# Kernel optimization log

Hardware: AMD Instinct MI355X
Metric: run time of the kernel (lower is better)

## Reference

```python
import jax, jax.numpy as jnp
import numpy as np
from jax import lax

CUTOFF = 0.25
SIGMA = 1.0
RADIUS = 4  # skimage/scipy default truncate=4.0 -> radius = round(4.0*sigma)


def _gauss_kernel(sigma=SIGMA, radius=RADIUS):
    x = np.arange(-radius, radius + 1, dtype=np.float32)
    k = np.exp(-0.5 * (x / sigma) ** 2)
    return jnp.asarray(k / k.sum())


def _blur_axis(x, axis, kernel):
    r = (kernel.shape[0] - 1) // 2
    pad = [(0, 0)] * x.ndim
    pad[axis] = (r, r)
    xp = jnp.pad(x, pad, mode='edge')  # scipy mode='nearest'
    out = jnp.zeros_like(x)
    for i in range(kernel.shape[0]):  # fixed small tap loop (9 taps)
        out = out + kernel[i] * lax.slice_in_dim(xp, i, i + x.shape[axis], axis=axis)
    return out


def gaussian_smoothing_4d(x):
    # skimage.filters.gaussian on a 4D array smooths over ALL axes (B, C, H, W)
    k = _gauss_kernel().astype(x.dtype)
    for ax in range(4):
        x = _blur_axis(x, ax, k)
    return x


def dht_2d(x):
    # real(FFT(x)) - imag(FFT(flip(x)))
    return (jnp.fft.fftn(x, axes=(2, 3)).real
            - jnp.fft.fftn(jnp.flip(x, axis=(2, 3)), axes=(2, 3)).imag).astype(x.dtype)


def _neg_k(a):
    # X_H(-k): flip both spatial mode axes, then roll by 1 (DC stays put)
    return jnp.roll(jnp.flip(a, axis=(-2, -1)), shift=(1, 1), axis=(-2, -1))


def compl_mul2d(x1, x2):
    x1n, x2n = _neg_k(x1), _neg_k(x2)
    e = lambda a, b: jnp.einsum('bixy,ioxy->boxy', a, b)
    return 0.5 * (e(x1, x2) - e(x1n, x2n) + e(x1, x2n) + e(x1n, x2))


def setup_inputs() -> dict:
    key = jax.random.key(0)
    k1, k2 = jax.random.split(key)
    B, Cin, Cout, H, W, M1, M2 = 16, 64, 64, 128, 128, 20, 20
    x = jax.random.normal(k1, (B, Cin, H, W), dtype=jnp.float32)
    scale = 1.0 / (Cin * Cout)
    w1 = scale * jax.random.uniform(k2, (Cin, Cout, M1, M2), dtype=jnp.float32)
    return {'x': x, 'w1': w1}


def reference(x, w1):
    B, _, H, W = x.shape
    Cout, M1, M2 = w1.shape[1], w1.shape[2], w1.shape[3]
    x_ht = dht_2d(x)
    out_ht = jnp.zeros((B, Cout, H, W), dtype=x.dtype)
    out_ht = out_ht.at[:, :, :M1, :M2].set(
        compl_mul2d(x_ht[:, :, :M1, :M2], w1))
    # inverse DHT = DHT / (H*W)
    y = dht_2d(out_ht) / (H * W)
    y = gaussian_smoothing_4d(y)
    # low-pass mask along last dim only (as in the original)
    freqs = jnp.fft.fftfreq(W)
    mask = (jnp.abs(freqs) <= CUTOFF).astype(y.dtype)
    return y * mask
```

## Files before the change

kernel.cpp:

```cpp
#include <hip/hip_runtime.h>


#define TWO_PI 6.283185307179586f
#define THETA (TWO_PI / 128.0f)

__device__ __forceinline__ void gauss9(float* g) {
  float s = 0.f;
#pragma unroll
  for (int t = 0; t < 9; ++t) { float d = (float)(t - 4); g[t] = expf(-0.5f * d * d); s += g[t]; }
  float inv = 1.f / s;
#pragma unroll
  for (int t = 0; t < 9; ++t) g[t] *= inv;
}

__global__ void __launch_bounds__(256, 4) kBig(
    const float* __restrict__ x, const float* __restrict__ w1,
    float* __restrict__ X1, float* __restrict__ wbT,
    float* __restrict__ L2g, float* __restrict__ RB2g) {
  __shared__ float lds[10240];
  int tid = threadIdx.x;
  int blk = blockIdx.x;

  if (blk >= 1024) {
    if (blk == 1472) {
      for (int i = tid; i < 5376; i += 256) {
        int u = i / 42, t = i - u * 42;
        int A = (t < 21) ? t : t - 21;
        float a = (float)((u * A) & 127) * THETA;
        lds[u * 44 + t] = (t < 21) ? cosf(a) : sinf(a);
      }
      __syncthreads();
      float g[9]; gauss9(g);
      for (int i = tid; i < 5376; i += 256) {
        int u = i / 42, t = i - u * 42;
        float acc = 0.f;
#pragma unroll
        for (int tp = 0; tp < 9; ++tp) {
          int uc = u - 4 + tp; uc = uc < 0 ? 0 : (uc > 127 ? 127 : uc);
          acc += g[tp] * lds[uc * 44 + t];
        }
        L2g[t * 128 + u] = acc;
        bool keep = (u <= 32) || (u >= 96);
        RB2g[t * 128 + u] = keep ? acc : 0.f;
      }
      return;
    }
    int bb = blk - 1024;
    int c = bb / 7, chunk = bb % 7;
    int m0 = chunk * 64;
    int mw = 400 - m0; if (mw > 64) mw = 64;
    for (int t = tid; t < 4096; t += 256) {
      int o = t >> 6, mm = t & 63;
      lds[o * 69 + mm] = (mm < mw) ? w1[(c * 64 + o) * 400 + m0 + mm] : 0.f;
    }
    __syncthreads();
    float g[9]; gauss9(g);
    for (int t = tid; t < 4096; t += 256) {
      int mm = t >> 6, o = t & 63;
      if (mm >= mw) continue;
      float acc = 0.f;
#pragma unroll
      for (int tp = 0; tp < 9; ++tp) {
        int oc = o - 4 + tp; oc = oc < 0 ? 0 : (oc > 63 ? 63 : oc);
        acc += g[tp] * lds[oc * 69 + mm];
      }
      wbT[(c * 400 + m0 + mm) * 64 + o] = acc;
    }
    return;
  }

  int bc = blk;
  const float* xb = x + (long)bc * 16384;

  for (int i = tid; i < 2600; i += 256) {
    int n2 = i / 40, col = i - n2 * 40;
    int k2 = (col < 20) ? col : col - 20;
    float s, c;
    sincosf((float)((k2 * n2) & 127) * THETA, &s, &c);
    lds[i] = (col < 20) ? c : s;
  }

  int rg = tid & 31, cg = tid >> 5;
  int r0 = rg * 4, c0 = cg * 5;
  float acc[4][5];
#pragma unroll
  for (int i = 0; i < 4; ++i)
#pragma unroll
    for (int j = 0; j < 5; ++j) acc[i][j] = 0.f;

  float* xsP = lds + 2600;
  float* xsM = lds + 4844;
  const float* xsrc = (cg < 4) ? xsP : xsM;

  for (int ch = 0; ch < 4; ++ch) {
    __syncthreads();
#pragma unroll
    for (int it = 0; it < 2; ++it) {
      int t = tid + it * 256;
      int n2l = t & 15, n1g = t >> 4;
      int base = ch * 16 + n2l;
      const float* gp = xb + n1g * 512 + base;
      float a0 = gp[0], a1 = gp[128], a2 = gp[256], a3 = gp[384];
      float b0 = 0.f, b1 = 0.f, b2 = 0.f, b3 = 0.f;
      if (base != 0) {
        const float* gm = xb + n1g * 512 + (128 - base);
        b0 = gm[0]; b1 = gm[128]; b2 = gm[256]; b3 = gm[384];
      }
      *(float4*)&xsP[n2l * 132 + n1g * 4] =
          make_float4(a0 + b0, a1 + b1, a2 + b2, a3 + b3);
      *(float4*)&xsM[n2l * 132 + n1g * 4] =
          make_float4(a0 - b0, a1 - b1, a2 - b2, a3 - b3);
    }
    if (ch == 3 && tid < 32) {
      int n1g = tid;
      const float* gp = xb + n1g * 512 + 64;
      float4 v = make_float4(gp[0], gp[128], gp[256], gp[384]);
      *(float4*)&xsP[16 * 132 + n1g * 4] = v;
      *(float4*)&xsM[16 * 132 + n1g * 4] = v;
    }
    __syncthreads();
#pragma unroll 4
    for (int k = 0; k < 16; ++k) {
      float4 av = *(const float4*)&xsrc[k * 132 + r0];
      const float* tr = lds + (ch * 16 + k) * 40 + c0;
      float bv[5] = {tr[0], tr[1], tr[2], tr[3], tr[4]};
      float avv[4] = {av.x, av.y, av.z, av.w};
#pragma unroll
      for (int i = 0; i < 4; ++i)
#pragma unroll
        for (int j = 0; j < 5; ++j) acc[i][j] += avv[i] * bv[j];
    }
    if (ch == 3) {
      float4 av = *(const float4*)&xsrc[16 * 132 + r0];
      const float* tr = lds + 64 * 40 + c0;
      float bv[5] = {tr[0], tr[1], tr[2], tr[3], tr[4]};
      float avv[4] = {av.x, av.y, av.z, av.w};
#pragma unroll
      for (int i = 0; i < 4; ++i)
#pragma unroll
        for (int j = 0; j < 5; ++j) acc[i][j] += avv[i] * bv[j];
    }
  }
  __syncthreads();
  for (int i = tid; i < 2560; i += 256) {
    int k1 = i >> 7, t = i & 127;
    float s, c;
    sincosf((float)((k1 * t) & 127) * THETA, &s, &c);
    lds[k1 * 128 + (t ^ ((k1 & 7) << 2))] = c;
    lds[(20 + k1) * 128 + (t ^ (((20 + k1) & 7) << 2))] = s;
  }
#pragma unroll
  for (int j = 0; j < 5; ++j) {
    int col = c0 + j;
    int k2 = (col < 20) ? col : col - 20;
    int part = (col < 20) ? 0 : 128;
    int m = (k2 & 7) << 2;
    *(float4*)&lds[5120 + k2 * 256 + ((part + r0) ^ m)] =
        make_float4(acc[0][j], acc[1][j], acc[2][j], acc[3][j]);
  }
  __syncthreads();
  if (tid < 200) {
    int k1 = tid / 10, k2 = (tid % 10) * 2;
    int mc = (k1 & 7) << 2, ms = ((20 + k1) & 7) << 2;
    int m0 = (k2 & 7) << 2, m1 = ((k2 + 1) & 7) << 2;
    const float* tgc = lds + k1 * 128;
    const float* tgs = lds + (20 + k1) * 128;
    const float* p0 = lds + 5120 + k2 * 256;
    const float* p1 = lds + 5120 + (k2 + 1) * 256;
    float Ac0 = 0.f, As0 = 0.f, Bc0 = 0.f, Bs0 = 0.f;
    float Ac1 = 0.f, As1 = 0.f, Bc1 = 0.f, Bs1 = 0.f;
    for (int t = 0; t < 128; t += 4) {
      float4 tc = *(const float4*)(tgc + (t ^ mc));
      float4 ts = *(const float4*)(tgs + (t ^ ms));
      float4 pc0 = *(const float4*)(p0 + (t ^ m0));
      float4 ps0 = *(const float4*)(p0 + 128 + (t ^ m0));
      float4 pc1 = *(const float4*)(p1 + (t ^ m1));
      float4 ps1 = *(const float4*)(p1 + 128 + (t ^ m1));
      Ac0 += tc.x*pc0.x + tc.y*pc0.y + tc.z*pc0.z + tc.w*pc0.w;
      As0 += ts.x*pc0.x + ts.y*pc0.y + ts.z*pc0.z + ts.w*pc0.w;
      Bc0 += tc.x*ps0.x + tc.y*ps0.y + tc.z*ps0.z + tc.w*ps0.w;
      Bs0 += ts.x*ps0.x + ts.y*ps0.y + ts.z*ps0.z + ts.w*ps0.w;
      Ac1 += tc.x*pc1.x + tc.y*pc1.y + tc.z*pc1.z + tc.w*pc1.w;
      As1 += ts.x*pc1.x + ts.y*pc1.y + ts.z*pc1.z + ts.w*pc1.w;
      Bc1 += tc.x*ps1.x + tc.y*ps1.y + tc.z*ps1.z + tc.w*ps1.w;
      Bs1 += ts.x*ps1.x + ts.y*ps1.y + ts.z*ps1.z + ts.w*ps1.w;
    }
    float sa, ca, sb, cb;
    sincosf(THETA * (float)(k1 + k2), &sa, &ca);
    sincosf(THETA * (float)(k1 + k2 + 1), &sb, &cb);
    X1[(k1 * 20 + k2) * 1024 + bc] = (Ac0 - Bs0) * (1.f - sa) - (As0 + Bc0) * ca;
    X1[(k1 * 20 + k2 + 1) * 1024 + bc] = (Ac1 - Bs1) * (1.f - sb) - (As1 + Bc1) * cb;
  }
}

__global__ void k3_mix(const float* __restrict__ X1, const float* __restrict__ wbT,
                       float* __restrict__ O) {
  __shared__ float Xp[16][64], Xm[16][64];
  int m = blockIdx.x;
  int i = m / 20, j = m - i * 20;
  int nm = ((20 - i) % 20) * 20 + ((20 - j) % 20);
  int tid = threadIdx.x;
  const float sc = 0.5f / 16384.0f;
  float g[9]; gauss9(g);
  {
    int bl = tid >> 6, c = tid & 63;
#pragma unroll
    for (int it = 0; it < 4; ++it) {
      int b = bl * 4 + it;
      float sa = 0.f, sn = 0.f;
#pragma unroll
      for (int tp = 0; tp < 9; ++tp) {
        int bb = b - 4 + tp; bb = bb < 0 ? 0 : (bb > 15 ? 15 : bb);
        sa += g[tp] * X1[m * 1024 + bb * 64 + c];
        sn += g[tp] * X1[nm * 1024 + bb * 64 + c];
      }
      Xp[b][c] = (sa + sn) * sc; Xm[b][c] = (sa - sn) * sc;
    }
  }
  __syncthreads();
  int o = tid & 63, bq = tid >> 6;
  float acc[4] = {0.f, 0.f, 0.f, 0.f};
#pragma unroll 4
  for (int c = 0; c < 64; ++c) {
    float wp = wbT[(c * 400 + m) * 64 + o];
    float wm = wbT[(c * 400 + nm) * 64 + o];
#pragma unroll
    for (int k = 0; k < 4; ++k)
      acc[k] += Xp[bq * 4 + k][c] * wp + Xm[bq * 4 + k][c] * wm;
  }
#pragma unroll
  for (int k = 0; k < 4; ++k)
    O[((bq * 4 + k) * 64 + o) * 400 + m] = acc[k];
}

__global__ void __launch_bounds__(256) k5b_final(const float* __restrict__ O,
                                                 const float* __restrict__ L2g,
                                                 const float* __restrict__ RB2g,
                                                 float* __restrict__ out) {
  __shared__ float Os[400];
  __shared__ float Rs[42 * 128];
  int bo = blockIdx.x, tid = threadIdx.x;
  for (int t = tid; t < 400; t += 256) Os[t] = O[bo * 400 + t];
  __syncthreads();
  const float4* Bc4 = (const float4*)RB2g;
  const float4* Bs4 = (const float4*)(RB2g + 21 * 128);
  {
    int rg = tid & 7;
    int vqIdx = tid >> 3;
    int vq = (vqIdx < 9) ? vqIdx : vqIdx + 15;
    if (rg < 7 && vqIdx < 17) {
      int r0 = rg * 6;
      float4 a[6];
#pragma unroll
      for (int q = 0; q < 6; ++q) a[q] = make_float4(0.f, 0.f, 0.f, 0.f);
      for (int k2 = 0; k2 <= 20; ++k2) {
        float4 bc4 = Bc4[k2 * 32 + vq];
        float4 bs4 = Bs4[k2 * 32 + vq];
#pragma unroll
        for (int q = 0; q < 6; ++q) {
          int r = r0 + q;
          bool isS = (r >= 21);
          int A = isS ? (r - 21) : r;
          if (k2 < 20 && A < 20) {
            float ov = Os[A * 20 + k2];
            const float4 b = isS ? bs4 : bc4;
            float s = isS ? -ov : ov;
            a[q].x += s * b.x; a[q].y += s * b.y; a[q].z += s * b.z; a[q].w += s * b.w;
          }
          if (k2 >= 1 && A >= 1) {
            float ov = Os[(A - 1) * 20 + (k2 - 1)];
            const float4 b = isS ? bc4 : bs4;
            a[q].x -= ov * b.x; a[q].y -= ov * b.y; a[q].z -= ov * b.z; a[q].w -= ov * b.w;
          }
        }
      }
#pragma unroll
      for (int q = 0; q < 6; ++q)
        *(float4*)&Rs[(r0 + q) * 128 + vq * 4] = a[q];
    }
  }
  __syncthreads();
  long base = (long)bo * 16384;
  {
    int half = tid >> 7;
    int uu = (tid >> 3) & 15;  int u0 = uu * 8;
    int vv = tid & 7;          int v0 = half ? (96 + vv * 4) : vv * 4;
    float acc[8][4];
#pragma unroll
    for (int a = 0; a < 8; ++a)
#pragma unroll
      for (int b = 0; b < 4; ++b) acc[a][b] = 0.f;
    for (int r = 0; r < 42; ++r) {
      float4 a0 = *(const float4*)(L2g + r * 128 + u0);
      float4 a1 = *(const float4*)(L2g + r * 128 + u0 + 4);
      float4 b0 = *(const float4*)&Rs[r * 128 + v0];
      float av[8] = {a0.x, a0.y, a0.z, a0.w, a1.x, a1.y, a1.z, a1.w};
      float bv[4] = {b0.x, b0.y, b0.z, b0.w};
#pragma unroll
      for (int a = 0; a < 8; ++a)
#pragma unroll
        for (int b = 0; b < 4; ++b) acc[a][b] += av[a] * bv[b];
    }
#pragma unroll
    for (int a = 0; a < 8; ++a)
      *(float4*)&out[base + (u0 + a) * 128 + v0] =
          make_float4(acc[a][0], acc[a][1], acc[a][2], acc[a][3]);
  }
  if (tid < 128) {
    float d = 0.f;
    for (int r = 0; r < 42; ++r) d += L2g[r * 128 + tid] * Rs[r * 128 + 32];
    out[base + tid * 128 + 32] = d;
  }
  float4 z4 = make_float4(0.f, 0.f, 0.f, 0.f);
  for (int jj = tid; jj < 2048; jj += 256) {
    int u = jj >> 4, s = jj & 15;
    long p = base + (long)u * 128;
    if (s == 15) { out[p + 33] = 0.f; out[p + 34] = 0.f; out[p + 35] = 0.f; }
    else *(float4*)&out[p + 36 + 4 * s] = z4;
  }
}

extern "C" void kernel_launch(void* const* d_in, const int* in_sizes, int n_in,
                              void* d_out, int out_size, void* d_ws, size_t ws_size,
                              hipStream_t stream) {
  const float* x = (const float*)d_in[0];
  const float* w1 = (const float*)d_in[1];
  float* out = (float*)d_out;
  float* ws = (float*)d_ws;

  float* X1 = ws;
  float* O = X1 + 409600;
  float* wbT = O + 409600;
  float* L2g = wbT + 1638400;
  float* RB2g = L2g + 5376;

  hipLaunchKernelGGL(kBig, dim3(1473), dim3(256), 0, stream,
                     x, w1, X1, wbT, L2g, RB2g);
  hipLaunchKernelGGL(k3_mix, dim3(400), dim3(256), 0, stream, X1, wbT, O);
  hipLaunchKernelGGL(k5b_final, dim3(1024), dim3(256), 0, stream, O, L2g, RB2g, out);
}
```

Before: 183.5 us.

## Transpose twiddle table for float4 loads and register-tile second-stage DFT across all threads

The first-stage twiddle table is stored transposed (column-major, stride 68), so each thread can fetch four consecutive k values per output column as a float4, cutting LDS load instructions in the row-transform inner loop. The second-stage 40x40 reduction over 128 points is now spread across all 256 threads. Each thread computes a 5x5 register tile over a quarter of the reduction range, writes the partials to LDS, and then 200 threads sum the four partial matrices. Before, only 200 threads each ran a serial 128-length dot product. The cost is an extra barrier, more registers, and an added LDS partial-sum pass.

Measured after the change: 590.2 us. 3.22x slower.

```diff
diff --git a/kernel.cpp b/kernel.cpp
--- a/kernel.cpp
+++ b/kernel.cpp
@@ -11,6 +11,10 @@
   float inv = 1.f / s;
 #pragma unroll
   for (int t = 0; t < 9; ++t) g[t] *= inv;
+}
+
+__device__ __forceinline__ float f4c(const float4& v, int kk) {
+  return kk == 0 ? v.x : kk == 1 ? v.y : kk == 2 ? v.z : v.w;
 }
 
 __global__ void __launch_bounds__(256, 4) kBig(
@@ -77,7 +81,7 @@
     int k2 = (col < 20) ? col : col - 20;
     float s, c;
     sincosf((float)((k2 * n2) & 127) * THETA, &s, &c);
-    lds[i] = (col < 20) ? c : s;
+    lds[col * 68 + n2] = (col < 20) ? c : s;
   }
 
   int rg = tid & 31, cg = tid >> 5;
@@ -88,8 +92,8 @@
 #pragma unroll
     for (int j = 0; j < 5; ++j) acc[i][j] = 0.f;
 
-  float* xsP = lds + 2600;
-  float* xsM = lds + 4844;
+  float* xsP = lds + 2720;
+  float* xsM = lds + 4964;
   const float* xsrc = (cg < 4) ? xsP : xsM;
 
   for (int ch = 0; ch < 4; ++ch) {
@@ -119,22 +123,28 @@
       *(float4*)&xsM[16 * 132 + n1g * 4] = v;
     }
     __syncthreads();
-#pragma unroll 4
-    for (int k = 0; k < 16; ++k) {
-      float4 av = *(const float4*)&xsrc[k * 132 + r0];
-      const float* tr = lds + (ch * 16 + k) * 40 + c0;
-      float bv[5] = {tr[0], tr[1], tr[2], tr[3], tr[4]};
-      float avv[4] = {av.x, av.y, av.z, av.w};
-#pragma unroll
-      for (int i = 0; i < 4; ++i)
-#pragma unroll
-        for (int j = 0; j < 5; ++j) acc[i][j] += avv[i] * bv[j];
+#pragma unroll
+    for (int k4 = 0; k4 < 4; ++k4) {
+      float4 bq[5];
+#pragma unroll
+      for (int j = 0; j < 5; ++j)
+        bq[j] = *(const float4*)&lds[(c0 + j) * 68 + ch * 16 + k4 * 4];
+#pragma unroll
+      for (int kk = 0; kk < 4; ++kk) {
+        float4 av = *(const float4*)&xsrc[(k4 * 4 + kk) * 132 + r0];
+        float avv[4] = {av.x, av.y, av.z, av.w};
+#pragma unroll
+        for (int i = 0; i < 4; ++i)
+#pragma unroll
+          for (int j = 0; j < 5; ++j) acc[i][j] += avv[i] * f4c(bq[j], kk);
+      }
     }
     if (ch == 3) {
       float4 av = *(const float4*)&xsrc[16 * 132 + r0];
-      const float* tr = lds + 64 * 40 + c0;
-      float bv[5] = {tr[0], tr[1], tr[2], tr[3], tr[4]};
       float avv[4] = {av.x, av.y, av.z, av.w};
+      float bv[5];
+#pragma unroll
+      for (int j = 0; j < 5; ++j) bv[j] = lds[(c0 + j) * 68 + 64];
 #pragma unroll
       for (int i = 0; i < 4; ++i)
 #pragma unroll
@@ -159,31 +169,57 @@
         make_float4(acc[0][j], acc[1][j], acc[2][j], acc[3][j]);
   }
   __syncthreads();
+  {
+    int nq = tid >> 6, rt = (tid >> 3) & 7, ct = tid & 7;
+    float acc2[5][5];
+#pragma unroll
+    for (int i = 0; i < 5; ++i)
+#pragma unroll
+      for (int j = 0; j < 5; ++j) acc2[i][j] = 0.f;
+    int t0 = nq * 32;
+#pragma unroll
+    for (int q = 0; q < 8; ++q) {
+      int t4 = t0 + q * 4;
+      float4 bb[5], aa[5];
+#pragma unroll
+      for (int i = 0; i < 5; ++i) {
+        int r = rt * 5 + i;
+        bb[i] = *(const float4*)&lds[r * 128 + (t4 ^ ((r & 7) << 2))];
+      }
+#pragma unroll
+      for (int j = 0; j < 5; ++j) {
+        int a = ct * 5 + j;
+        int k2 = (a < 20) ? a : a - 20;
+        int part = (a < 20) ? 0 : 128;
+        int m = (k2 & 7) << 2;
+        aa[j] = *(const float4*)&lds[5120 + k2 * 256 + ((part + t4) ^ m)];
+      }
+#pragma unroll
+      for (int i = 0; i < 5; ++i)
+#pragma unroll
+        for (int j = 0; j < 5; ++j)
+          acc2[i][j] += bb[i].x * aa[j].x + bb[i].y * aa[j].y
+                      + bb[i].z * aa[j].z + bb[i].w * aa[j].w;
+    }
+    __syncthreads();
+#pragma unroll
+    for (int i = 0; i < 5; ++i)
+#pragma unroll
+      for (int j = 0; j < 5; ++j)
+        lds[nq * 1640 + (rt * 5 + i) * 41 + (ct * 5 + j)] = acc2[i][j];
+  }
+  __syncthreads();
   if (tid < 200) {
     int k1 = tid / 10, k2 = (tid % 10) * 2;
-    int mc = (k1 & 7) << 2, ms = ((20 + k1) & 7) << 2;
-    int m0 = (k2 & 7) << 2, m1 = ((k2 + 1) & 7) << 2;
-    const float* tgc = lds + k1 * 128;
-    const float* tgs = lds + (20 + k1) * 128;
-    const float* p0 = lds + 5120 + k2 * 256;
-    const float* p1 = lds + 5120 + (k2 + 1) * 256;
     float Ac0 = 0.f, As0 = 0.f, Bc0 = 0.f, Bs0 = 0.f;
     float Ac1 = 0.f, As1 = 0.f, Bc1 = 0.f, Bs1 = 0.f;
-    for (int t = 0; t < 128; t += 4) {
-      float4 tc = *(const float4*)(tgc + (t ^ mc));
-      float4 ts = *(const float4*)(tgs + (t ^ ms));
-      float4 pc0 = *(const float4*)(p0 + (t ^ m0));
-      float4 ps0 = *(const float4*)(p0 + 128 + (t ^ m0));
-      float4 pc1 = *(const float4*)(p1 + (t ^ m1));
-      float4 ps1 = *(const float4*)(p1 + 128 + (t ^ m1));
-      Ac0 += tc.x*pc0.x + tc.y*pc0.y + tc.z*pc0.z + tc.w*pc0.w;
-      As0 += ts.x*pc0.x + ts.y*pc0.y + ts.z*pc0.z + ts.w*pc0.w;
-      Bc0 += tc.x*ps0.x + tc.y*ps0.y + tc.z*ps0.z + tc.w*ps0.w;
-      Bs0 += ts.x*ps0.x + ts.y*ps0.y + ts.z*ps0.z + ts.w*ps0.w;
-      Ac1 += tc.x*pc1.x + tc.y*pc1.y + tc.z*pc1.z + tc.w*pc1.w;
-      As1 += ts.x*pc1.x + ts.y*pc1.y + ts.z*pc1.z + ts.w*pc1.w;
-      Bc1 += tc.x*ps1.x + tc.y*ps1.y + tc.z*ps1.z + tc.w*ps1.w;
-      Bs1 += ts.x*ps1.x + ts.y*ps1.y + ts.z*ps1.z + ts.w*ps1.w;
+#pragma unroll
+    for (int nq = 0; nq < 4; ++nq) {
+      const float* Mb = lds + nq * 1640;
+      Ac0 += Mb[k1 * 41 + k2];            As0 += Mb[(20 + k1) * 41 + k2];
+      Bc0 += Mb[k1 * 41 + 20 + k2];       Bs0 += Mb[(20 + k1) * 41 + 20 + k2];
+      Ac1 += Mb[k1 * 41 + k2 + 1];        As1 += Mb[(20 + k1) * 41 + k2 + 1];
+      Bc1 += Mb[k1 * 41 + 21 + k2];       Bs1 += Mb[(20 + k1) * 41 + 21 + k2];
     }
     float sa, ca, sb, cb;
     sincosf(THETA * (float)(k1 + k2), &sa, &ca);
```
